# Optimization experiments

Hardware: AMD Instinct MI355X
Metric: run time of the kernel (lower is better)

## Reference

```python
import jax, jax.numpy as jnp
import numpy as np

B, N, DIM = 2, 2048, 1024
NUM_HEADS = 16
EFF = NUM_HEADS // 2          # 8 effective heads
HD = DIM // NUM_HEADS         # 64
LAMBDA_INIT = 0.8
EPS = 1e-5


def setup_inputs() -> dict:
    key = jax.random.key(0)
    ks = jax.random.split(key, 16)
    s = 0.02
    return {
        "x":  jax.random.normal(ks[0], (B, N, DIM), dtype=jnp.float32),
        "Wq": jax.random.normal(ks[1], (DIM, DIM), dtype=jnp.float32) * s,
        "bq": jnp.zeros((DIM,), dtype=jnp.float32),
        "Wk": jax.random.normal(ks[2], (DIM, DIM), dtype=jnp.float32) * s,
        "bk": jnp.zeros((DIM,), dtype=jnp.float32),
        "Wv": jax.random.normal(ks[3], (DIM, DIM), dtype=jnp.float32) * s,
        "bv": jnp.zeros((DIM,), dtype=jnp.float32),
        "Wo": jax.random.normal(ks[4], (DIM, DIM), dtype=jnp.float32) * s,
        "bo": jnp.zeros((DIM,), dtype=jnp.float32),
        "norm_w": jnp.ones((2 * HD,), dtype=jnp.float32),
        "lq1": jax.random.normal(ks[5], (HD,), dtype=jnp.float32) * 0.1,
        "lk1": jax.random.normal(ks[6], (HD,), dtype=jnp.float32) * 0.1,
        "lq2": jax.random.normal(ks[7], (HD,), dtype=jnp.float32) * 0.1,
        "lk2": jax.random.normal(ks[8], (HD,), dtype=jnp.float32) * 0.1,
    }


def reference(x, Wq, bq, Wk, bk, Wv, bv, Wo, bo, norm_w, lq1, lk1, lq2, lk2):
    scale = HD ** -0.5
    # projections (torch Linear: y = x @ W.T + b)
    q = (x @ Wq.T + bq).reshape(B, N, NUM_HEADS, HD).transpose(0, 2, 1, 3) * scale  # [B,2E,N,hd]
    k = (x @ Wk.T + bk).reshape(B, N, NUM_HEADS, HD).transpose(0, 2, 1, 3)          # [B,2E,N,hd]
    v = (x @ Wv.T + bv).reshape(B, N, EFF, 2 * HD).transpose(0, 2, 1, 3)            # [B,E,N,2hd]

    scores = jnp.einsum('bhqd,bhkd->bhqk', q, k)              # [B,2E,N,N]
    probs = jax.nn.softmax(scores, axis=-1)
    probs = probs.reshape(B, EFF, 2, N, N)                    # pair consecutive heads

    lam = jnp.exp(jnp.sum(lq1 * lk1)) - jnp.exp(jnp.sum(lq2 * lk2)) + LAMBDA_INIT
    diff = probs[:, :, 0] - lam * probs[:, :, 1]              # [B,E,N,N]

    out = jnp.einsum('behk,bekd->behd'.replace('e','h').replace('hh','h') if False else 'bhqk,bhkd->bhqd', diff, v)  # [B,E,N,2hd]
    # headwise RMSNorm over last dim (2*hd)
    out = out * jax.lax.rsqrt(jnp.mean(out * out, axis=-1, keepdims=True) + EPS) * norm_w
    out = out * (1.0 - LAMBDA_INIT)

    out = out.transpose(0, 2, 1, 3).reshape(B, N, DIM)
    return out @ Wo.T + bo
```

## Files before the change

kernel.cpp:

```cpp
#include <hip/hip_runtime.h>
#include <hip/hip_bf16.h>

#define B_   2
#define N_   2048
#define DIM_ 1024
#define HD_  64
#define DV_  128

typedef __bf16 bf16;
typedef __bf16 bf16x8 __attribute__((ext_vector_type(8)));
typedef __bf16 bf16x4 __attribute__((ext_vector_type(4)));
typedef float  floatx4 __attribute__((ext_vector_type(4)));

#if __has_builtin(__builtin_amdgcn_exp2f)
#define EXP2(x) __builtin_amdgcn_exp2f(x)
#else
#define EXP2(x) exp2f(x)
#endif

#define QSCALE 0.1803368801111244f

__device__ __forceinline__ void async16(const void* g, void* l) {
  __builtin_amdgcn_global_load_lds(
      (__attribute__((address_space(1))) void*)g,
      (__attribute__((address_space(3))) void*)l, 16, 0, 0);
}

__global__ void convert_kernel(const float* __restrict__ x,
                               const float* __restrict__ wq,
                               const float* __restrict__ wk,
                               const float* __restrict__ wv,
                               const float* __restrict__ wo,
                               bf16* __restrict__ dst) {
  const int NX = B_ * N_ * DIM_;
  const int NW = DIM_ * DIM_;
  int i = (blockIdx.x * 256 + threadIdx.x) * 4;
  const float* src;
  int off;
  if (i < NX) { src = x; off = i; }
  else {
    int j = i - NX;
    int w = j >> 20;
    off = j & (NW - 1);
    src = (w == 0) ? wq : (w == 1) ? wk : (w == 2) ? wv : wo;
  }
  float4 v = *(const float4*)(src + off);
  bf16x4 o = { (bf16)v.x, (bf16)v.y, (bf16)v.z, (bf16)v.w };
  *(bf16x4*)(dst + i) = o;
}

__global__ void lam_kernel(const float* __restrict__ lq1, const float* __restrict__ lk1,
                           const float* __restrict__ lq2, const float* __restrict__ lk2,
                           float* __restrict__ lam_out) {
  int l = threadIdx.x;
  float a = lq1[l] * lk1[l];
  float b = lq2[l] * lk2[l];
  for (int m = 1; m < 64; m <<= 1) {
    a += __shfl_xor(a, m, 64);
    b += __shfl_xor(b, m, 64);
  }
  if (l == 0) *lam_out = __expf(a) - __expf(b) + 0.8f;
}

__global__ __launch_bounds__(256) void proj_kernel(
    const bf16* __restrict__ xb, const bf16* __restrict__ wall,
    const float* __restrict__ bq, const float* __restrict__ bk,
    const float* __restrict__ bv,
    bf16* __restrict__ qo, bf16* __restrict__ ko, bf16* __restrict__ vt) {
  __shared__ __align__(16) bf16 At[128 * 64];
  __shared__ __align__(16) bf16 Bt[128 * 64];
  const int tid = threadIdx.x, lane = tid & 63, w = tid >> 6;
  const int tm = blockIdx.x, tn = blockIdx.y, z = blockIdx.z;
  const int quad = lane >> 4, l15 = lane & 15;
  const int wm = (w >> 1) * 64, wn = (w & 1) * 64;
  const bf16* Ab = xb + (long)tm * 128 * DIM_;
  const bf16* Bb = wall + (long)z * (DIM_ * DIM_) + (long)tn * 128 * DIM_;
  floatx4 zero = {0.f, 0.f, 0.f, 0.f};
  floatx4 acc[4][4];
#pragma unroll
  for (int i = 0; i < 4; ++i)
#pragma unroll
    for (int j = 0; j < 4; ++j) acc[i][j] = zero;

  for (int kb = 0; kb < DIM_ / 64; ++kb) {
    for (int idx = tid; idx < 1024; idx += 256) {
      int row = idx >> 3, ch = idx & 7, g = ch ^ (row & 7);
      async16(Ab + row * DIM_ + kb * 64 + g * 8, (char*)At + (idx - lane) * 16);
      async16(Bb + row * DIM_ + kb * 64 + g * 8, (char*)Bt + (idx - lane) * 16);
    }
    __syncthreads();
#pragma unroll
    for (int ks = 0; ks < 2; ++ks) {
      bf16x8 af[4], bfm[4];
#pragma unroll
      for (int mt = 0; mt < 4; ++mt) {
        int r = wm + mt * 16 + l15;
        af[mt] = *(const bf16x8*)&At[r * 64 + ((ks * 4 + quad) ^ (r & 7)) * 8];
      }
#pragma unroll
      for (int nt = 0; nt < 4; ++nt) {
        int r = wn + nt * 16 + l15;
        bfm[nt] = *(const bf16x8*)&Bt[r * 64 + ((ks * 4 + quad) ^ (r & 7)) * 8];
      }
#pragma unroll
      for (int mt = 0; mt < 4; ++mt)
#pragma unroll
        for (int nt = 0; nt < 4; ++nt)
          acc[mt][nt] = __builtin_amdgcn_mfma_f32_16x16x32_bf16(
              af[mt], bfm[nt], acc[mt][nt], 0, 0, 0);
    }
    __syncthreads();
  }
#pragma unroll
  for (int mt = 0; mt < 4; ++mt)
#pragma unroll
    for (int nt = 0; nt < 4; ++nt)
#pragma unroll
      for (int r = 0; r < 4; ++r) {
        int grow = tm * 128 + wm + mt * 16 + quad * 4 + r;
        int gcol = tn * 128 + wn + nt * 16 + l15;
        float v = acc[mt][nt][r];
        if (z == 0) {
          qo[(long)grow * DIM_ + gcol] = (bf16)((v + bq[gcol]) * QSCALE);
        } else if (z == 1) {
          ko[(long)grow * DIM_ + gcol] = (bf16)(v + bk[gcol]);
        } else {
          int bb = grow >> 11, key = grow & (N_ - 1);
          int e = gcol >> 7, d = gcol & 127;
          vt[(((long)(bb * 8 + e)) * DV_ + d) * N_ + key] = (bf16)(v + bv[gcol]);
        }
      }
}

__global__ __launch_bounds__(256, 2) void attn_kernel(
    const bf16* __restrict__ qb, const bf16* __restrict__ kbuf,
    const bf16* __restrict__ vt, const float* __restrict__ lamp,
    const float* __restrict__ norm_w, bf16* __restrict__ ao) {
  __shared__ __align__(16) bf16 Kt[2][2 * 64 * 64];
  __shared__ __align__(16) bf16 Vt[2][128 * 64];
  __shared__ __align__(16) bf16 Pt[4][2][16 * 64];

  const int tid = threadIdx.x, lane = tid & 63, w = tid >> 6;
  const int qt = blockIdx.x, e = blockIdx.y, b = blockIdx.z;
  const int quad = lane >> 4, l15 = lane & 15;
  floatx4 zero = {0.f, 0.f, 0.f, 0.f};

  const int qrow = qt * 64 + w * 16 + l15;
  const bf16* qrp = qb + (long)(b * N_ + qrow) * DIM_ + e * 128;
  bf16x8 qf0[2], qf1[2];
  qf0[0] = *(const bf16x8*)(qrp + quad * 8);
  qf0[1] = *(const bf16x8*)(qrp + 32 + quad * 8);
  qf1[0] = *(const bf16x8*)(qrp + 64 + quad * 8);
  qf1[1] = *(const bf16x8*)(qrp + 96 + quad * 8);

  const bf16* kbase = kbuf + (long)b * N_ * DIM_ + e * 128;
  const bf16* vbase = vt + (long)(b * 8 + e) * DV_ * N_;

  floatx4 acc0[8], acc1[8];
#pragma unroll
  for (int i = 0; i < 8; ++i) { acc0[i] = zero; acc1[i] = zero; }
  float lp0[4] = {0.f, 0.f, 0.f, 0.f};
  float lp1[4] = {0.f, 0.f, 0.f, 0.f};

  bf16* Pt0 = Pt[w][0];
  bf16* Pt1 = Pt[w][1];

#define STAGE(ktv, bufv)                                                            \
  {                                                                                 \
    int kt_ = (ktv), buf_ = (bufv);                                                 \
    _Pragma("unroll") for (int t = 0; t < 4; ++t) {                                 \
      int idx = tid + t * 256;                                                      \
      int khl = idx >> 9, row = (idx >> 3) & 63, ch = idx & 7, g = ch ^ (row & 7);  \
      async16(kbase + ((long)(kt_ * 64 + row)) * DIM_ + khl * 64 + g * 8,           \
              (char*)Kt[buf_] + (idx - lane) * 16);                                 \
    }                                                                               \
    _Pragma("unroll") for (int t = 0; t < 4; ++t) {                                 \
      int idx = tid + t * 256;                                                      \
      int row = idx >> 3, ch = idx & 7, g = ch ^ (row & 7);                         \
      async16(vbase + (long)row * N_ + kt_ * 64 + g * 8,                            \
              (char*)Vt[buf_] + (idx - lane) * 16);                                 \
    }                                                                               \
  }

  STAGE(0, 0);

  for (int kt = 0; kt < N_ / 64; ++kt) {
    const int buf = kt & 1;
    __syncthreads();
    if (kt + 1 < N_ / 64) STAGE(kt + 1, buf ^ 1);

    const bf16* Kh0 = Kt[buf];
    const bf16* Kh1 = Kt[buf] + 4096;
    const bf16* Vb = Vt[buf];

    floatx4 s0[4], s1[4];
#pragma unroll
    for (int nt = 0; nt < 4; ++nt) { s0[nt] = zero; s1[nt] = zero; }
#pragma unroll
    for (int ks = 0; ks < 2; ++ks) {
#pragma unroll
      for (int nt = 0; nt < 4; ++nt) {
        int br = nt * 16 + l15;
        int so = ((ks * 4 + quad) ^ (br & 7)) * 8;
        bf16x8 b0 = *(const bf16x8*)&Kh0[br * 64 + so];
        bf16x8 b1 = *(const bf16x8*)&Kh1[br * 64 + so];
        s0[nt] = __builtin_amdgcn_mfma_f32_16x16x32_bf16(qf0[ks], b0, s0[nt], 0, 0, 0);
        s1[nt] = __builtin_amdgcn_mfma_f32_16x16x32_bf16(qf1[ks], b1, s1[nt], 0, 0, 0);
      }
    }

#pragma unroll
    for (int r = 0; r < 4; ++r) {
      int row = quad * 4 + r;
      int a0 = row * 64 + ((l15 >> 3) ^ (row & 7)) * 8 + (l15 & 7);
      int a1 = row * 64 + (((16 + l15) >> 3) ^ (row & 7)) * 8 + (l15 & 7);
      int a2 = row * 64 + (((32 + l15) >> 3) ^ (row & 7)) * 8 + (l15 & 7);
      int a3 = row * 64 + (((48 + l15) >> 3) ^ (row & 7)) * 8 + (l15 & 7);
      float p0 = EXP2(s0[0][r]), p1 = EXP2(s0[1][r]);
      float p2 = EXP2(s0[2][r]), p3 = EXP2(s0[3][r]);
      lp0[r] += (p0 + p1) + (p2 + p3);
      Pt0[a0] = (bf16)p0; Pt0[a1] = (bf16)p1; Pt0[a2] = (bf16)p2; Pt0[a3] = (bf16)p3;
      float u0 = EXP2(s1[0][r]), u1 = EXP2(s1[1][r]);
      float u2 = EXP2(s1[2][r]), u3 = EXP2(s1[3][r]);
      lp1[r] += (u0 + u1) + (u2 + u3);
      Pt1[a0] = (bf16)u0; Pt1[a1] = (bf16)u1; Pt1[a2] = (bf16)u2; Pt1[a3] = (bf16)u3;
    }

#pragma unroll
    for (int ks = 0; ks < 2; ++ks) {
      int ao_ = l15 * 64 + ((ks * 4 + quad) ^ (l15 & 7)) * 8;
      bf16x8 af0 = *(const bf16x8*)&Pt0[ao_];
      bf16x8 af1 = *(const bf16x8*)&Pt1[ao_];
#pragma unroll
      for (int dt = 0; dt < 8; ++dt) {
        int br = dt * 16 + l15;
        bf16x8 bfm = *(const bf16x8*)&Vb[br * 64 + ((ks * 4 + quad) ^ (br & 7)) * 8];
        acc0[dt] = __builtin_amdgcn_mfma_f32_16x16x32_bf16(af0, bfm, acc0[dt], 0, 0, 0);
        acc1[dt] = __builtin_amdgcn_mfma_f32_16x16x32_bf16(af1, bfm, acc1[dt], 0, 0, 0);
      }
    }
  }

  float inv0[4], inv1[4];
#pragma unroll
  for (int r = 0; r < 4; ++r) {
    float a = lp0[r], c = lp1[r];
#pragma unroll
    for (int msk = 1; msk < 16; msk <<= 1) {
      a += __shfl_xor(a, msk, 16);
      c += __shfl_xor(c, msk, 16);
    }
    inv0[r] = 1.0f / a;
    inv1[r] = 1.0f / c;
  }

  float lam = *lamp;
  float ss[4] = {0.f, 0.f, 0.f, 0.f};
#pragma unroll
  for (int dt = 0; dt < 8; ++dt)
#pragma unroll
    for (int r = 0; r < 4; ++r) {
      float v = acc0[dt][r] * inv0[r] - lam * (acc1[dt][r] * inv1[r]);
      acc0[dt][r] = v;
      ss[r] += v * v;
    }
  float rms[4];
#pragma unroll
  for (int r = 0; r < 4; ++r) {
    float t = ss[r];
#pragma unroll
    for (int msk = 1; msk < 16; msk <<= 1) t += __shfl_xor(t, msk, 16);
    rms[r] = rsqrtf(t * (1.0f / 128.0f) + 1e-5f);
  }
#pragma unroll
  for (int dt = 0; dt < 8; ++dt) {
    float nwv = norm_w[dt * 16 + l15] * 0.2f;
#pragma unroll
    for (int r = 0; r < 4; ++r) {
      int n = qt * 64 + w * 16 + quad * 4 + r;
      ao[((long)(b * N_ + n)) * DIM_ + e * DV_ + dt * 16 + l15] =
          (bf16)(acc0[dt][r] * rms[r] * nwv);
    }
  }
}

__global__ __launch_bounds__(256) void out_gemm(
    const bf16* __restrict__ ab, const bf16* __restrict__ wo,
    const float* __restrict__ bo, float* __restrict__ out) {
  __shared__ __align__(16) bf16 At[128 * 64];
  __shared__ __align__(16) bf16 Bt[128 * 64];
  const int tid = threadIdx.x, lane = tid & 63, w = tid >> 6;
  const int tm = blockIdx.x, tn = blockIdx.y;
  const int quad = lane >> 4, l15 = lane & 15;
  const int wm = (w >> 1) * 64, wn = (w & 1) * 64;
  const bf16* Ab = ab + (long)tm * 128 * DIM_;
  const bf16* Bb = wo + (long)tn * 128 * DIM_;
  floatx4 zero = {0.f, 0.f, 0.f, 0.f};
  floatx4 acc[4][4];
#pragma unroll
  for (int i = 0; i < 4; ++i)
#pragma unroll
    for (int j = 0; j < 4; ++j) acc[i][j] = zero;

  for (int kb = 0; kb < DIM_ / 64; ++kb) {
    for (int idx = tid; idx < 1024; idx += 256) {
      int row = idx >> 3, ch = idx & 7, g = ch ^ (row & 7);
      async16(Ab + row * DIM_ + kb * 64 + g * 8, (char*)At + (idx - lane) * 16);
      async16(Bb + row * DIM_ + kb * 64 + g * 8, (char*)Bt + (idx - lane) * 16);
    }
    __syncthreads();
#pragma unroll
    for (int ks = 0; ks < 2; ++ks) {
      bf16x8 af[4], bfm[4];
#pragma unroll
      for (int mt = 0; mt < 4; ++mt) {
        int r = wm + mt * 16 + l15;
        af[mt] = *(const bf16x8*)&At[r * 64 + ((ks * 4 + quad) ^ (r & 7)) * 8];
      }
#pragma unroll
      for (int nt = 0; nt < 4; ++nt) {
        int r = wn + nt * 16 + l15;
        bfm[nt] = *(const bf16x8*)&Bt[r * 64 + ((ks * 4 + quad) ^ (r & 7)) * 8];
      }
#pragma unroll
      for (int mt = 0; mt < 4; ++mt)
#pragma unroll
        for (int nt = 0; nt < 4; ++nt)
          acc[mt][nt] = __builtin_amdgcn_mfma_f32_16x16x32_bf16(
              af[mt], bfm[nt], acc[mt][nt], 0, 0, 0);
    }
    __syncthreads();
  }
#pragma unroll
  for (int mt = 0; mt < 4; ++mt)
#pragma unroll
    for (int nt = 0; nt < 4; ++nt)
#pragma unroll
      for (int r = 0; r < 4; ++r) {
        int grow = tm * 128 + wm + mt * 16 + quad * 4 + r;
        int gcol = tn * 128 + wn + nt * 16 + l15;
        out[(long)grow * DIM_ + gcol] = acc[mt][nt][r] + bo[gcol];
      }
}

extern "C" void kernel_launch(void* const* d_in, const int* in_sizes, int n_in,
                              void* d_out, int out_size, void* d_ws, size_t ws_size,
                              hipStream_t stream) {
  const float* x    = (const float*)d_in[0];
  const float* Wq   = (const float*)d_in[1];
  const float* bq   = (const float*)d_in[2];
  const float* Wk   = (const float*)d_in[3];
  const float* bk   = (const float*)d_in[4];
  const float* Wv   = (const float*)d_in[5];
  const float* bv   = (const float*)d_in[6];
  const float* Wo   = (const float*)d_in[7];
  const float* bo   = (const float*)d_in[8];
  const float* nw   = (const float*)d_in[9];
  const float* lq1  = (const float*)d_in[10];
  const float* lk1  = (const float*)d_in[11];
  const float* lq2  = (const float*)d_in[12];
  const float* lk2  = (const float*)d_in[13];

  char* ws = (char*)d_ws;
  float* lam = (float*)ws;
  bf16* xb   = (bf16*)(ws + 256);
  bf16* wqb  = xb + 4194304;
  bf16* qb   = wqb + 4 * 1048576;
  bf16* kbuf = qb + 4194304;
  bf16* vtb  = kbuf + 4194304;
  bf16* ab   = vtb + 4194304;

  convert_kernel<<<8192, 256, 0, stream>>>(x, Wq, Wk, Wv, Wo, xb);
  lam_kernel<<<1, 64, 0, stream>>>(lq1, lk1, lq2, lk2, lam);
  proj_kernel<<<dim3(32, 8, 3), 256, 0, stream>>>(xb, wqb, bq, bk, bv, qb, kbuf, vtb);
  attn_kernel<<<dim3(32, 8, 2), 256, 0, stream>>>(qb, kbuf, vtb, lam, nw, ab);
  out_gemm<<<dim3(32, 8), 256, 0, stream>>>(ab, wqb + 3 * 1048576, bo, (float*)d_out);
}
```

Measured before the change: 239.8 us.

## Compute transposed scores to vectorize P stores and stage V transpose through LDS

The attention QK^T MFMA swaps operands so each lane holds four consecutive keys for one query row. Probabilities can then be written to LDS as packed bf16x4 with an XOR swizzle instead of scalar stores, and row sums reduce across quads with a shuffle at the end. The projection kernel's V output is transposed through shared memory so global writes to the [d, key] layout become coalesced 16-byte stores instead of strided scalar writes. This adds an extra LDS round trip and a barrier in the V path, and changes the swizzle patterns, which risks bank conflicts.

```diff
diff --git a/kernel.cpp b/kernel.cpp
--- a/kernel.cpp
+++ b/kernel.cpp
@@ -67,8 +67,9 @@
     const float* __restrict__ bq, const float* __restrict__ bk,
     const float* __restrict__ bv,
     bf16* __restrict__ qo, bf16* __restrict__ ko, bf16* __restrict__ vt) {
-  __shared__ __align__(16) bf16 At[128 * 64];
-  __shared__ __align__(16) bf16 Bt[128 * 64];
+  __shared__ __align__(16) bf16 SM[2 * 128 * 64];
+  bf16* At = SM;
+  bf16* Bt = SM + 128 * 64;
   const int tid = threadIdx.x, lane = tid & 63, w = tid >> 6;
   const int tm = blockIdx.x, tn = blockIdx.y, z = blockIdx.z;
   const int quad = lane >> 4, l15 = lane & 15;
@@ -111,25 +112,49 @@
     }
     __syncthreads();
   }
-#pragma unroll
-  for (int mt = 0; mt < 4; ++mt)
-#pragma unroll
-    for (int nt = 0; nt < 4; ++nt)
-#pragma unroll
-      for (int r = 0; r < 4; ++r) {
-        int grow = tm * 128 + wm + mt * 16 + quad * 4 + r;
-        int gcol = tn * 128 + wn + nt * 16 + l15;
-        float v = acc[mt][nt][r];
-        if (z == 0) {
-          qo[(long)grow * DIM_ + gcol] = (bf16)((v + bq[gcol]) * QSCALE);
-        } else if (z == 1) {
-          ko[(long)grow * DIM_ + gcol] = (bf16)(v + bk[gcol]);
-        } else {
-          int bb = grow >> 11, key = grow & (N_ - 1);
-          int e = gcol >> 7, d = gcol & 127;
-          vt[(((long)(bb * 8 + e)) * DV_ + d) * N_ + key] = (bf16)(v + bv[gcol]);
+
+  if (z != 2) {
+#pragma unroll
+    for (int mt = 0; mt < 4; ++mt)
+#pragma unroll
+      for (int nt = 0; nt < 4; ++nt)
+#pragma unroll
+        for (int r = 0; r < 4; ++r) {
+          int grow = tm * 128 + wm + mt * 16 + quad * 4 + r;
+          int gcol = tn * 128 + wn + nt * 16 + l15;
+          float v = acc[mt][nt][r];
+          if (z == 0) {
+            qo[(long)grow * DIM_ + gcol] = (bf16)((v + bq[gcol]) * QSCALE);
+          } else {
+            ko[(long)grow * DIM_ + gcol] = (bf16)(v + bk[gcol]);
+          }
         }
-      }
+  } else {
+    bf16* Vl = SM;
+#pragma unroll
+    for (int nt = 0; nt < 4; ++nt) {
+      int d = wn + nt * 16 + l15;
+      float bvv = bv[tn * 128 + d];
+      int m = (d & 7) * 2;
+#pragma unroll
+      for (int mt = 0; mt < 4; ++mt) {
+        bf16x4 v4 = { (bf16)(acc[mt][nt][0] + bvv), (bf16)(acc[mt][nt][1] + bvv),
+                      (bf16)(acc[mt][nt][2] + bvv), (bf16)(acc[mt][nt][3] + bvv) };
+        int c = (wm >> 2) + mt * 4 + quad;
+        *(bf16x4*)&Vl[d * 128 + (c ^ m) * 4] = v4;
+      }
+    }
+    __syncthreads();
+    const int bb = tm >> 4, e = tn;
+    const long rowbase = ((long)(bb * 8 + e) * 128) * (long)N_ + (tm & 15) * 128;
+#pragma unroll
+    for (int p = 0; p < 8; ++p) {
+      int d = p * 16 + (tid >> 4), j = tid & 15;
+      int cs = (2 * j) ^ ((d & 7) * 2);
+      bf16x8 val = *(const bf16x8*)&Vl[d * 128 + cs * 4];
+      *(bf16x8*)&vt[rowbase + (long)d * N_ + j * 8] = val;
+    }
+  }
 }
 
 __global__ __launch_bounds__(256, 2) void attn_kernel(
@@ -159,8 +184,7 @@
   floatx4 acc0[8], acc1[8];
 #pragma unroll
   for (int i = 0; i < 8; ++i) { acc0[i] = zero; acc1[i] = zero; }
-  float lp0[4] = {0.f, 0.f, 0.f, 0.f};
-  float lp1[4] = {0.f, 0.f, 0.f, 0.f};
+  float lp0 = 0.f, lp1 = 0.f;
 
   bf16* Pt0 = Pt[w][0];
   bf16* Pt1 = Pt[w][1];
@@ -202,35 +226,37 @@
       for (int nt = 0; nt < 4; ++nt) {
         int br = nt * 16 + l15;
         int so = ((ks * 4 + quad) ^ (br & 7)) * 8;
-        bf16x8 b0 = *(const bf16x8*)&Kh0[br * 64 + so];
-        bf16x8 b1 = *(const bf16x8*)&Kh1[br * 64 + so];
-        s0[nt] = __builtin_amdgcn_mfma_f32_16x16x32_bf16(qf0[ks], b0, s0[nt], 0, 0, 0);
-        s1[nt] = __builtin_amdgcn_mfma_f32_16x16x32_bf16(qf1[ks], b1, s1[nt], 0, 0, 0);
-      }
-    }
-
-#pragma unroll
-    for (int r = 0; r < 4; ++r) {
-      int row = quad * 4 + r;
-      int a0 = row * 64 + ((l15 >> 3) ^ (row & 7)) * 8 + (l15 & 7);
-      int a1 = row * 64 + (((16 + l15) >> 3) ^ (row & 7)) * 8 + (l15 & 7);
-      int a2 = row * 64 + (((32 + l15) >> 3) ^ (row & 7)) * 8 + (l15 & 7);
-      int a3 = row * 64 + (((48 + l15) >> 3) ^ (row & 7)) * 8 + (l15 & 7);
-      float p0 = EXP2(s0[0][r]), p1 = EXP2(s0[1][r]);
-      float p2 = EXP2(s0[2][r]), p3 = EXP2(s0[3][r]);
-      lp0[r] += (p0 + p1) + (p2 + p3);
-      Pt0[a0] = (bf16)p0; Pt0[a1] = (bf16)p1; Pt0[a2] = (bf16)p2; Pt0[a3] = (bf16)p3;
-      float u0 = EXP2(s1[0][r]), u1 = EXP2(s1[1][r]);
-      float u2 = EXP2(s1[2][r]), u3 = EXP2(s1[3][r]);
-      lp1[r] += (u0 + u1) + (u2 + u3);
-      Pt1[a0] = (bf16)u0; Pt1[a1] = (bf16)u1; Pt1[a2] = (bf16)u2; Pt1[a3] = (bf16)u3;
+        bf16x8 k0 = *(const bf16x8*)&Kh0[br * 64 + so];
+        bf16x8 k1 = *(const bf16x8*)&Kh1[br * 64 + so];
+        s0[nt] = __builtin_amdgcn_mfma_f32_16x16x32_bf16(k0, qf0[ks], s0[nt], 0, 0, 0);
+        s1[nt] = __builtin_amdgcn_mfma_f32_16x16x32_bf16(k1, qf1[ks], s1[nt], 0, 0, 0);
+      }
+    }
+
+#pragma unroll
+    for (int nt = 0; nt < 4; ++nt) {
+      float p0 = EXP2(s0[nt][0]), p1 = EXP2(s0[nt][1]);
+      float p2 = EXP2(s0[nt][2]), p3 = EXP2(s0[nt][3]);
+      lp0 += (p0 + p1) + (p2 + p3);
+      bf16x4 v0 = { (bf16)p0, (bf16)p1, (bf16)p2, (bf16)p3 };
+      int c = nt * 4 + quad;
+      *(bf16x4*)&Pt0[l15 * 64 + (c ^ l15) * 4] = v0;
+      float u0 = EXP2(s1[nt][0]), u1 = EXP2(s1[nt][1]);
+      float u2 = EXP2(s1[nt][2]), u3 = EXP2(s1[nt][3]);
+      lp1 += (u0 + u1) + (u2 + u3);
+      bf16x4 v1 = { (bf16)u0, (bf16)u1, (bf16)u2, (bf16)u3 };
+      *(bf16x4*)&Pt1[l15 * 64 + (c ^ l15) * 4] = v1;
     }
 
 #pragma unroll
     for (int ks = 0; ks < 2; ++ks) {
-      int ao_ = l15 * 64 + ((ks * 4 + quad) ^ (l15 & 7)) * 8;
-      bf16x8 af0 = *(const bf16x8*)&Pt0[ao_];
-      bf16x8 af1 = *(const bf16x8*)&Pt1[ao_];
+      int c0 = 8 * ks + 2 * quad;
+      bf16x4 a0lo = *(const bf16x4*)&Pt0[l15 * 64 + ((c0) ^ l15) * 4];
+      bf16x4 a0hi = *(const bf16x4*)&Pt0[l15 * 64 + ((c0 + 1) ^ l15) * 4];
+      bf16x4 a1lo = *(const bf16x4*)&Pt1[l15 * 64 + ((c0) ^ l15) * 4];
+      bf16x4 a1hi = *(const bf16x4*)&Pt1[l15 * 64 + ((c0 + 1) ^ l15) * 4];
+      bf16x8 af0 = __builtin_shufflevector(a0lo, a0hi, 0, 1, 2, 3, 4, 5, 6, 7);
+      bf16x8 af1 = __builtin_shufflevector(a1lo, a1hi, 0, 1, 2, 3, 4, 5, 6, 7);
 #pragma unroll
       for (int dt = 0; dt < 8; ++dt) {
         int br = dt * 16 + l15;
@@ -241,17 +267,15 @@
     }
   }
 
+  lp0 += __shfl_xor(lp0, 16, 64);
+  lp0 += __shfl_xor(lp0, 32, 64);
+  lp1 += __shfl_xor(lp1, 16, 64);
+  lp1 += __shfl_xor(lp1, 32, 64);
   float inv0[4], inv1[4];
 #pragma unroll
   for (int r = 0; r < 4; ++r) {
-    float a = lp0[r], c = lp1[r];
-#pragma unroll
-    for (int msk = 1; msk < 16; msk <<= 1) {
-      a += __shfl_xor(a, msk, 16);
-      c += __shfl_xor(c, msk, 16);
-    }
-    inv0[r] = 1.0f / a;
-    inv1[r] = 1.0f / c;
+    inv0[r] = 1.0f / __shfl(lp0, quad * 4 + r, 64);
+    inv1[r] = 1.0f / __shfl(lp1, quad * 4 + r, 64);
   }
 
   float lam = *lamp;
```

Result: faster. 223.3 us (-6.9%).
